# Performance work log

Measured on AMD Instinct MI355X. Metric: run time of the kernel, lower is better.

Reference implementation:

```python
import jax, jax.numpy as jnp
import numpy as np

DIM = 384
HEADS = 6
HEAD_DIM = DIM // HEADS
MLP_DIM = int(DIM * 4.0)
EPS = 1e-5


def layer_norm(x, g, b):
    mu = jnp.mean(x, axis=-1, keepdims=True)
    var = jnp.mean(jnp.square(x - mu), axis=-1, keepdims=True)
    return (x - mu) * jax.lax.rsqrt(var + EPS) * g + b


def setup_inputs() -> dict:
    key = jax.random.key(0)
    ks = jax.random.split(key, 12)
    s = 0.02
    return {
        "x": jax.random.normal(ks[0], (8, 2048, DIM), dtype=jnp.float32),
        "ln1_g": jnp.ones((DIM,), jnp.float32),
        "ln1_b": jnp.zeros((DIM,), jnp.float32),
        "qkv_w": jax.random.normal(ks[1], (DIM, 3 * DIM), jnp.float32) * s,
        "qkv_b": jnp.zeros((3 * DIM,), jnp.float32),
        "proj_w": jax.random.normal(ks[2], (DIM, DIM), jnp.float32) * s,
        "proj_b": jnp.zeros((DIM,), jnp.float32),
        "ln2_g": jnp.ones((DIM,), jnp.float32),
        "ln2_b": jnp.zeros((DIM,), jnp.float32),
        "fc1_w": jax.random.normal(ks[3], (DIM, MLP_DIM), jnp.float32) * s,
        "fc1_b": jnp.zeros((MLP_DIM,), jnp.float32),
        "fc2_w": jax.random.normal(ks[4], (MLP_DIM, DIM), jnp.float32) * s,
        "fc2_b": jnp.zeros((DIM,), jnp.float32),
    }


def reference(x, ln1_g, ln1_b, qkv_w, qkv_b, proj_w, proj_b,
              ln2_g, ln2_b, fc1_w, fc1_b, fc2_w, fc2_b):
    B, N, C = x.shape
    # --- attention ---
    h = layer_norm(x, ln1_g, ln1_b)
    qkv = h @ qkv_w + qkv_b  # [B,N,3C]
    qkv = qkv.reshape(B, N, 3, HEADS, HEAD_DIM)
    q, k, v = jnp.moveaxis(qkv, 2, 0)  # each [B,N,H,D]
    scale = HEAD_DIM ** -0.5
    attn = jnp.einsum('bnhd,bmhd->bhnm', q, k) * scale  # [B,H,N,N]
    attn = jax.nn.softmax(attn, axis=-1)
    o = jnp.einsum('bhnm,bmhd->bnhd', attn, v).reshape(B, N, C)
    x = x + o @ proj_w + proj_b
    # --- mlp ---
    h = layer_norm(x, ln2_g, ln2_b)
    h = jax.nn.gelu(h @ fc1_w + fc1_b, approximate=False)
    x = x + h @ fc2_w + fc2_b
    return x
```

## Files before the change

kernel.cpp:

```cpp
#include <hip/hip_runtime.h>
#include <hip/hip_bf16.h>

#define DIM   384
#define SEQ   2048
#define BATCH 8
#define NHEAD 6
#define HD    64
#define MLPD  1536
#define MTOT  (BATCH*SEQ)

typedef __attribute__((ext_vector_type(8))) short bf16x8;
typedef __attribute__((ext_vector_type(4))) float f32x4;

static __device__ __forceinline__ float bf2f(unsigned short u){
    union { float f; unsigned int i; } v; v.i = ((unsigned int)u) << 16; return v.f;
}
static __device__ __forceinline__ unsigned short f2bf(float f){
    union { float f; unsigned int i; } v; v.f = f;
    unsigned int r = v.i + 0x7fffu + ((v.i >> 16) & 1u);
    return (unsigned short)(r >> 16);
}
static __device__ __forceinline__ unsigned int asu(float f){
    union { float f; unsigned int i; } v; v.f = f; return v.i;
}
static __device__ __forceinline__ void gload_lds16(const unsigned short* g, unsigned short* l){
    __builtin_amdgcn_global_load_lds(
        (__attribute__((address_space(1))) void*)(g),
        (__attribute__((address_space(3))) void*)(l), 16, 0, 0);
}

__global__ __launch_bounds__(256) void wt_all_kernel(
    const float* __restrict__ qkv_w, const float* __restrict__ proj_w,
    const float* __restrict__ fc1_w, const float* __restrict__ fc2_w,
    unsigned short* __restrict__ o_qkv, unsigned short* __restrict__ o_prj,
    unsigned short* __restrict__ o_fc1, unsigned short* __restrict__ o_fc2)
{
    __shared__ float tile[64][68];
    int bid = blockIdx.x;
    const float* W; unsigned short* Wt; int K, N, tk, tn;
    if (bid < 108)      { W = qkv_w; Wt = o_qkv; K = 384;  N = 1152; tk = bid/18;        tn = bid%18; }
    else if (bid < 144) { W = proj_w; Wt = o_prj; K = 384;  N = 384;  tk = (bid-108)/6;  tn = (bid-108)%6; }
    else if (bid < 288) { W = fc1_w; Wt = o_fc1; K = 384;  N = 1536; tk = (bid-144)/24; tn = (bid-144)%24; }
    else                { W = fc2_w; Wt = o_fc2; K = 1536; N = 384;  tk = (bid-288)/6;  tn = (bid-288)%6; }
    int t = threadIdx.x;
    int lr = t >> 4, lc = (t & 15) * 4;
#pragma unroll
    for (int p = 0; p < 4; p++){
        float4 v = *(const float4*)(W + (size_t)(tk*64 + p*16 + lr) * N + tn*64 + lc);
        *(float4*)&tile[p*16 + lr][lc] = v;
    }
    __syncthreads();
    int n = t >> 2, k0 = (t & 3) * 16;
    unsigned int w[8];
#pragma unroll
    for (int i = 0; i < 8; i++)
        w[i] = (unsigned int)f2bf(tile[k0 + 2*i][n]) | ((unsigned int)f2bf(tile[k0 + 2*i + 1][n]) << 16);
    unsigned short* dst = Wt + (size_t)(tn*64 + n) * K + tk*64 + k0;
    *(uint4*)(dst)     = make_uint4(w[0], w[1], w[2], w[3]);
    *(uint4*)(dst + 8) = make_uint4(w[4], w[5], w[6], w[7]);
}

__global__ __launch_bounds__(256) void vt_kernel(const unsigned short* __restrict__ vtmp,
                                                 unsigned short* __restrict__ vb){
    __shared__ unsigned short tile[64][72];
    int bh = blockIdx.y, ns0 = blockIdx.x * 64;
    const unsigned short* src = vtmp + ((size_t)bh * SEQ + ns0) * 64;
    int t = threadIdx.x;
#pragma unroll
    for (int p = 0; p < 2; p++){
        int idx = t + p * 256;
        int r = idx >> 3, c = (idx & 7) * 8;
        *(uint4*)&tile[r][c] = *(const uint4*)(src + (size_t)r * 64 + c);
    }
    __syncthreads();
    int d = t >> 2, j0 = (t & 3) * 16;
    unsigned int w[8];
#pragma unroll
    for (int m = 0; m < 8; m++)
        w[m] = (unsigned int)tile[j0 + 2*m][d] | ((unsigned int)tile[j0 + 2*m + 1][d] << 16);
    unsigned short* dst = vb + ((size_t)bh * 64 + d) * SEQ + ns0 + j0;
    *(uint4*)(dst)     = make_uint4(w[0], w[1], w[2], w[3]);
    *(uint4*)(dst + 8) = make_uint4(w[4], w[5], w[6], w[7]);
}

__global__ __launch_bounds__(256) void ln_kernel(const float* __restrict__ x,
                                                 const float* __restrict__ g,
                                                 const float* __restrict__ b,
                                                 unsigned short* __restrict__ out){
    int row  = blockIdx.x * 4 + (threadIdx.x >> 6);
    int lane = threadIdx.x & 63;
    const float* xr = x + (size_t)row * DIM;
    float v[6];
#pragma unroll
    for (int p = 0; p < 3; p++){
        float2 t = *(const float2*)(xr + lane * 2 + p * 128);
        v[2*p] = t.x; v[2*p+1] = t.y;
    }
    float s = 0.f, sq = 0.f;
#pragma unroll
    for (int i = 0; i < 6; i++){ s += v[i]; sq += v[i] * v[i]; }
#pragma unroll
    for (int off = 1; off < 64; off <<= 1){
        s  += __shfl_xor(s, off);
        sq += __shfl_xor(sq, off);
    }
    float mu   = s * (1.0f / DIM);
    float var  = sq * (1.0f / DIM) - mu * mu;
    float rstd = rsqrtf(var + 1e-5f);
    unsigned short* orow = out + (size_t)row * DIM;
#pragma unroll
    for (int p = 0; p < 3; p++){
        int c = lane * 2 + p * 128;
        float h0 = (v[2*p]   - mu) * rstd * g[c]   + b[c];
        float h1 = (v[2*p+1] - mu) * rstd * g[c+1] + b[c+1];
        unsigned int pk = (unsigned int)f2bf(h0) | ((unsigned int)f2bf(h1) << 16);
        *(unsigned int*)(orow + c) = pk;
    }
}

template<int EPI, int BN>
__global__ __launch_bounds__(256) void gemm_kernel(
    const unsigned short* __restrict__ A, const unsigned short* __restrict__ Bt,
    const float* __restrict__ bias, int K, int N,
    const float* __restrict__ resid, float* __restrict__ outf,
    unsigned short* __restrict__ outb,
    unsigned short* __restrict__ qb, unsigned short* __restrict__ kb2,
    unsigned short* __restrict__ vb)
{
    constexpr int FI = (BN == 128) ? 4 : 2;
    constexpr int WROWS = (BN == 128) ? 64 : 32;
    __shared__ __align__(16) unsigned short As[128 * 64];
    __shared__ __align__(16) unsigned short Bs[BN * 64];
    int t = threadIdx.x;
    int wid = t >> 6, lane = t & 63, quad = lane >> 4, l15 = lane & 15;
    int wr = (BN == 128) ? (wid >> 1) : wid;
    int wc = (BN == 128) ? (wid & 1) : 0;
    int row0 = blockIdx.y * 128, col0 = blockIdx.x * BN;
    int sr = lane >> 3, sc = lane & 7;
    int scl = (sc ^ sr) * 8;

    const unsigned short* Ab = A  + (size_t)row0 * K;
    const unsigned short* Bb = Bt + (size_t)col0 * K;

    f32x4 acc[FI][4];
    f32x4 zz = {0.f, 0.f, 0.f, 0.f};
#pragma unroll
    for (int i = 0; i < FI; i++)
#pragma unroll
        for (int j = 0; j < 4; j++) acc[i][j] = zz;

    for (int k0 = 0; k0 < K; k0 += 64){
        __syncthreads();
#pragma unroll
        for (int j = 0; j < 4; j++){
            int rb = wid * 32 + j * 8;
            gload_lds16(Ab + (size_t)(rb + sr) * K + k0 + scl, &As[rb * 64]);
            if (BN == 128){
                gload_lds16(Bb + (size_t)(rb + sr) * K + k0 + scl, &Bs[rb * 64]);
            } else if (j < 2){
                int rb2 = wid * 16 + j * 8;
                gload_lds16(Bb + (size_t)(rb2 + sr) * K + k0 + scl, &Bs[rb2 * 64]);
            }
        }
        __syncthreads();
#pragma unroll
        for (int kk = 0; kk < 2; kk++){
            bf16x8 af[FI], bf[4];
#pragma unroll
            for (int i = 0; i < FI; i++){
                int r = wr*WROWS + i*16 + l15;
                af[i] = *(const bf16x8*)&As[r * 64 + (((kk*4 + quad) ^ (l15 & 7)) * 8)];
            }
#pragma unroll
            for (int j = 0; j < 4; j++){
                int r = wc*64 + j*16 + l15;
                bf[j] = *(const bf16x8*)&Bs[r * 64 + (((kk*4 + quad) ^ (l15 & 7)) * 8)];
            }
#pragma unroll
            for (int i = 0; i < FI; i++)
#pragma unroll
                for (int j = 0; j < 4; j++)
                    acc[i][j] = __builtin_amdgcn_mfma_f32_16x16x32_bf16(af[i], bf[j], acc[i][j], 0, 0, 0);
        }
    }

#pragma unroll
    for (int i = 0; i < FI; i++){
#pragma unroll
        for (int j = 0; j < 4; j++){
            int gr0 = row0 + wr*WROWS + i*16 + quad*4;
            int gc  = col0 + wc*64 + j*16 + l15;
            float bia = bias[gc];
#pragma unroll
            for (int r = 0; r < 4; r++){
                int gr = gr0 + r;
                float val = acc[i][j][r] + bia;
                if (EPI == 1){
                    outf[(size_t)gr * N + gc] = resid[(size_t)gr * N + gc] + val;
                } else if (EPI == 2){
                    float u = val * (1.0f + 0.044715f * val * val);
                    float e = __builtin_amdgcn_exp2f(u * 2.3025851f);
                    outb[(size_t)gr * N + gc] = f2bf(val * e / (e + 1.0f));
                } else {
                    int trip = gc / 384, rem = gc - trip * 384;
                    int head = rem >> 6, d = rem & 63;
                    int bidx = gr >> 11, ns = gr & 2047;
                    size_t off = ((size_t)(bidx * NHEAD + head) * SEQ + ns) * 64 + d;
                    unsigned short* dst = (trip == 0) ? qb : (trip == 1) ? kb2 : vb;
                    dst[off] = f2bf(val);
                }
            }
        }
    }
}

__global__ __launch_bounds__(128, 3) void attn_kernel(const unsigned short* __restrict__ Q,
                                                      const unsigned short* __restrict__ Kb,
                                                      const unsigned short* __restrict__ Vt,
                                                      unsigned short* __restrict__ O){
    __shared__ __align__(16) unsigned short Ks[64 * 64];
    __shared__ __align__(16) unsigned short Vs[64 * 64];
    __shared__ __align__(16) unsigned short Ps[2][32 * 64];

    int bh = blockIdx.y, qt = blockIdx.x;
    int t = threadIdx.x, wid = t >> 6, lane = t & 63, quad = lane >> 4, l15 = lane & 15;
    int l7 = l15 & 7;
    int q0 = qt * 64 + wid * 32;
    const unsigned short* Qp = Q  + (size_t)bh * SEQ * 64;
    const unsigned short* Kp = Kb + (size_t)bh * SEQ * 64;
    const unsigned short* Vp = Vt + (size_t)bh * 64 * SEQ;
    int sr = lane >> 3, sc = lane & 7;
    int scl = (sc ^ sr) * 8;

    const float QSCALE = 0.125f * 1.44269504f;
    bf16x8 qf[2][2];
#pragma unroll
    for (int h = 0; h < 2; h++){
#pragma unroll
        for (int c = 0; c < 2; c++){
            union { uint4 u; unsigned short s[8]; } cv;
            cv.u = *(const uint4*)(Qp + (size_t)(q0 + h*16 + l15) * 64 + c * 32 + quad * 8);
            bf16x8 f;
#pragma unroll
            for (int j = 0; j < 8; j++) f[j] = (short)f2bf(bf2f(cv.s[j]) * QSCALE);
            qf[h][c] = f;
        }
    }

    bf16x8 ones;
#pragma unroll
    for (int j = 0; j < 8; j++) ones[j] = (short)0x3F80;

    f32x4 oacc[2][4], sacc[2];
    f32x4 zz = {0.f, 0.f, 0.f, 0.f};
#pragma unroll
    for (int h = 0; h < 2; h++){
        sacc[h] = zz;
#pragma unroll
        for (int dn = 0; dn < 4; dn++) oacc[h][dn] = zz;
    }
    unsigned short* P = &Ps[wid][0];

    const unsigned short* kf_ptr[4][2];
#pragma unroll
    for (int n = 0; n < 4; n++){
        int kv = n * 16 + l15;
        kf_ptr[n][0] = &Ks[kv * 64 + ((quad       ^ (kv & 7)) * 8)];
        kf_ptr[n][1] = &Ks[kv * 64 + (((4 + quad) ^ (kv & 7)) * 8)];
    }
    const unsigned short* vf_ptr[2][4];
#pragma unroll
    for (int c = 0; c < 2; c++)
#pragma unroll
        for (int dn = 0; dn < 4; dn++){
            int d = dn * 16 + l15;
            vf_ptr[c][dn] = &Vs[d * 64 + (((c*4 + quad) ^ (d & 7)) * 8)];
        }
    const unsigned short* pf_ptr[2][2];
#pragma unroll
    for (int c = 0; c < 2; c++)
#pragma unroll
        for (int h = 0; h < 2; h++)
            pf_ptr[c][h] = P + (h*16 + l15) * 64 + (((c*4 + quad) ^ l7) * 8);
    uint2* pw_ptr[2][4];
#pragma unroll
    for (int h = 0; h < 2; h++)
#pragma unroll
        for (int n = 0; n < 4; n++){
            int qloc = h * 16 + l15;
            int chunk = n * 2 + (quad >> 1);
            pw_ptr[h][n] = (uint2*)(P + qloc * 64 + ((chunk ^ l7) * 8) + (quad & 1) * 4);
        }
    const unsigned short* kstage[4];
    const unsigned short* vstage[4];
    unsigned short* klds[4];
    unsigned short* vlds[4];
#pragma unroll
    for (int jj = 0; jj < 4; jj++){
        int rb = wid * 32 + jj * 8;
        kstage[jj] = Kp + (size_t)(rb + sr) * 64 + scl;
        vstage[jj] = Vp + (size_t)(rb + sr) * SEQ + scl;
        klds[jj] = &Ks[rb * 64];
        vlds[jj] = &Vs[rb * 64];
    }

    for (int kt = 0; kt < SEQ / 64; kt++){
        __syncthreads();
#pragma unroll
        for (int jj = 0; jj < 4; jj++){
            gload_lds16(kstage[jj], klds[jj]);
            gload_lds16(vstage[jj], vlds[jj]);
            kstage[jj] += 64 * 64;
            vstage[jj] += 64;
        }
        __syncthreads();

        f32x4 st[2][4];
#pragma unroll
        for (int n = 0; n < 4; n++){
            bf16x8 kf0 = *(const bf16x8*)kf_ptr[n][0];
            bf16x8 kf1 = *(const bf16x8*)kf_ptr[n][1];
#pragma unroll
            for (int h = 0; h < 2; h++){
                f32x4 z = __builtin_amdgcn_mfma_f32_16x16x32_bf16(kf0, qf[h][0], zz, 0, 0, 0);
                st[h][n] = __builtin_amdgcn_mfma_f32_16x16x32_bf16(kf1, qf[h][1], z, 0, 0, 0);
            }
        }

#pragma unroll
        for (int h = 0; h < 2; h++){
#pragma unroll
            for (int n = 0; n < 4; n++){
                float p0 = __builtin_amdgcn_exp2f(st[h][n][0]);
                float p1 = __builtin_amdgcn_exp2f(st[h][n][1]);
                float p2 = __builtin_amdgcn_exp2f(st[h][n][2]);
                float p3 = __builtin_amdgcn_exp2f(st[h][n][3]);
                unsigned int w0 = __builtin_amdgcn_perm(asu(p1), asu(p0), 0x07060302u);
                unsigned int w1 = __builtin_amdgcn_perm(asu(p3), asu(p2), 0x07060302u);
                *pw_ptr[h][n] = make_uint2(w0, w1);
            }
        }

        asm volatile("s_waitcnt lgkmcnt(0)" ::: "memory");

#pragma unroll
        for (int c = 0; c < 2; c++){
            bf16x8 pf[2];
#pragma unroll
            for (int h = 0; h < 2; h++)
                pf[h] = *(const bf16x8*)pf_ptr[c][h];
            sacc[0] = __builtin_amdgcn_mfma_f32_16x16x32_bf16(ones, pf[0], sacc[0], 0, 0, 0);
            sacc[1] = __builtin_amdgcn_mfma_f32_16x16x32_bf16(ones, pf[1], sacc[1], 0, 0, 0);
#pragma unroll
            for (int dn = 0; dn < 4; dn++){
                bf16x8 vf = *(const bf16x8*)vf_ptr[c][dn];
                oacc[0][dn] = __builtin_amdgcn_mfma_f32_16x16x32_bf16(vf, pf[0], oacc[0][dn], 0, 0, 0);
                oacc[1][dn] = __builtin_amdgcn_mfma_f32_16x16x32_bf16(vf, pf[1], oacc[1][dn], 0, 0, 0);
            }
        }
    }

    int b = bh / NHEAD, hh = bh - b * NHEAD;
#pragma unroll
    for (int h = 0; h < 2; h++){
        float rd = 1.0f / sacc[h][0];
        size_t row = (size_t)(b * SEQ + q0 + h*16 + l15);
#pragma unroll
        for (int dn = 0; dn < 4; dn++){
            float v0 = oacc[h][dn][0] * rd, v1 = oacc[h][dn][1] * rd;
            float v2 = oacc[h][dn][2] * rd, v3 = oacc[h][dn][3] * rd;
            unsigned int w0 = (unsigned int)f2bf(v0) | ((unsigned int)f2bf(v1) << 16);
            unsigned int w1 = (unsigned int)f2bf(v2) | ((unsigned int)f2bf(v3) << 16);
            *(uint2*)(O + row * DIM + hh * 64 + dn * 16 + quad * 4) = make_uint2(w0, w1);
        }
    }
}

extern "C" void kernel_launch(void* const* d_in, const int* in_sizes, int n_in,
                              void* d_out, int out_size, void* d_ws, size_t ws_size,
                              hipStream_t stream){
    const float* x      = (const float*)d_in[0];
    const float* ln1_g  = (const float*)d_in[1];
    const float* ln1_b  = (const float*)d_in[2];
    const float* qkv_w  = (const float*)d_in[3];
    const float* qkv_b  = (const float*)d_in[4];
    const float* proj_w = (const float*)d_in[5];
    const float* proj_b = (const float*)d_in[6];
    const float* ln2_g  = (const float*)d_in[7];
    const float* ln2_b  = (const float*)d_in[8];
    const float* fc1_w  = (const float*)d_in[9];
    const float* fc1_b  = (const float*)d_in[10];
    const float* fc2_w  = (const float*)d_in[11];
    const float* fc2_b  = (const float*)d_in[12];
    float* out = (float*)d_out;

    char* p = (char*)d_ws;
    auto take = [&](size_t n){ char* r = p; p += (n + 255) & ~(size_t)255; return r; };
    unsigned short* wt_qkv = (unsigned short*)take((size_t)1152 * 384 * 2);
    unsigned short* wt_prj = (unsigned short*)take((size_t)384 * 384 * 2);
    unsigned short* wt_fc1 = (unsigned short*)take((size_t)1536 * 384 * 2);
    unsigned short* wt_fc2 = (unsigned short*)take((size_t)384 * 1536 * 2);
    unsigned short* rbig   = (unsigned short*)take((size_t)MTOT * 4 * DIM * 2);
    unsigned short* h2     = (unsigned short*)take((size_t)MTOT * DIM * 2);
    float*          x1     = (float*)take((size_t)MTOT * DIM * 4);

    unsigned short* h1     = rbig;
    unsigned short* qb     = rbig + (size_t)MTOT * DIM;
    unsigned short* kb     = qb   + (size_t)MTOT * DIM;
    unsigned short* vb     = kb   + (size_t)MTOT * DIM;
    unsigned short* vtmp   = h2;
    unsigned short* attn_o = rbig;
    unsigned short* hm     = rbig;

    wt_all_kernel<<<dim3(432), 256, 0, stream>>>(qkv_w, proj_w, fc1_w, fc2_w,
                                                 wt_qkv, wt_prj, wt_fc1, wt_fc2);
    ln_kernel<<<dim3(MTOT/4), 256, 0, stream>>>(x, ln1_g, ln1_b, h1);
    gemm_kernel<0,128><<<dim3(9, 128), 256, 0, stream>>>(h1, wt_qkv, qkv_b, 384, 1152,
                                                         nullptr, nullptr, nullptr, qb, kb, vtmp);
    vt_kernel<<<dim3(SEQ/64, BATCH*NHEAD), 256, 0, stream>>>(vtmp, vb);
    attn_kernel<<<dim3(SEQ/64, BATCH*NHEAD), 128, 0, stream>>>(qb, kb, vb, attn_o);
    gemm_kernel<1,64><<<dim3(6, 128), 256, 0, stream>>>(attn_o, wt_prj, proj_b, 384, 384,
                                                        x, x1, nullptr, nullptr, nullptr, nullptr);
    ln_kernel<<<dim3(MTOT/4), 256, 0, stream>>>(x1, ln2_g, ln2_b, h2);
    gemm_kernel<2,128><<<dim3(12, 128), 256, 0, stream>>>(h2, wt_fc1, fc1_b, 384, 1536,
                                                          nullptr, nullptr, hm, nullptr, nullptr, nullptr);
    gemm_kernel<1,64><<<dim3(6, 128), 256, 0, stream>>>(hm, wt_fc2, fc2_b, 1536, 384,
                                                        x1, out, nullptr, nullptr, nullptr, nullptr);
}
```

Before: 329.5 us.

## Fuse V transpose into QKV GEMM epilogue and retile GEMMs to 64x128

Removes the separate vt_kernel by having QKV GEMM blocks that cover V columns stage their output in shared memory transposed and write it directly in [bh][d][seq] layout. All GEMMs are retiled to 64x128 tiles with 128-thread blocks and launch bounds of 3 blocks per CU, each wave computing 32x128. This saves one kernel launch plus a full round trip of V through global memory, at the cost of higher register use per thread and smaller blocks.

```diff
diff --git a/kernel.cpp b/kernel.cpp
--- a/kernel.cpp
+++ b/kernel.cpp
@@ -60,29 +60,6 @@
     *(uint4*)(dst + 8) = make_uint4(w[4], w[5], w[6], w[7]);
 }
 
-__global__ __launch_bounds__(256) void vt_kernel(const unsigned short* __restrict__ vtmp,
-                                                 unsigned short* __restrict__ vb){
-    __shared__ unsigned short tile[64][72];
-    int bh = blockIdx.y, ns0 = blockIdx.x * 64;
-    const unsigned short* src = vtmp + ((size_t)bh * SEQ + ns0) * 64;
-    int t = threadIdx.x;
-#pragma unroll
-    for (int p = 0; p < 2; p++){
-        int idx = t + p * 256;
-        int r = idx >> 3, c = (idx & 7) * 8;
-        *(uint4*)&tile[r][c] = *(const uint4*)(src + (size_t)r * 64 + c);
-    }
-    __syncthreads();
-    int d = t >> 2, j0 = (t & 3) * 16;
-    unsigned int w[8];
-#pragma unroll
-    for (int m = 0; m < 8; m++)
-        w[m] = (unsigned int)tile[j0 + 2*m][d] | ((unsigned int)tile[j0 + 2*m + 1][d] << 16);
-    unsigned short* dst = vb + ((size_t)bh * 64 + d) * SEQ + ns0 + j0;
-    *(uint4*)(dst)     = make_uint4(w[0], w[1], w[2], w[3]);
-    *(uint4*)(dst + 8) = make_uint4(w[4], w[5], w[6], w[7]);
-}
-
 __global__ __launch_bounds__(256) void ln_kernel(const float* __restrict__ x,
                                                  const float* __restrict__ g,
                                                  const float* __restrict__ b,
@@ -118,8 +95,8 @@
     }
 }
 
-template<int EPI, int BN>
-__global__ __launch_bounds__(256) void gemm_kernel(
+template<int EPI>
+__global__ __launch_bounds__(128, 3) void gemm_kernel(
     const unsigned short* __restrict__ A, const unsigned short* __restrict__ Bt,
     const float* __restrict__ bias, int K, int N,
     const float* __restrict__ resid, float* __restrict__ outf,
@@ -127,69 +104,91 @@
     unsigned short* __restrict__ qb, unsigned short* __restrict__ kb2,
     unsigned short* __restrict__ vb)
 {
-    constexpr int FI = (BN == 128) ? 4 : 2;
-    constexpr int WROWS = (BN == 128) ? 64 : 32;
-    __shared__ __align__(16) unsigned short As[128 * 64];
-    __shared__ __align__(16) unsigned short Bs[BN * 64];
+    __shared__ __align__(16) unsigned short smem[64*64 + 128*64];
+    unsigned short* As = smem;
+    unsigned short* Bs = smem + 64*64;
     int t = threadIdx.x;
     int wid = t >> 6, lane = t & 63, quad = lane >> 4, l15 = lane & 15;
-    int wr = (BN == 128) ? (wid >> 1) : wid;
-    int wc = (BN == 128) ? (wid & 1) : 0;
-    int row0 = blockIdx.y * 128, col0 = blockIdx.x * BN;
+    int row0 = blockIdx.y * 64, col0 = blockIdx.x * 128;
     int sr = lane >> 3, sc = lane & 7;
     int scl = (sc ^ sr) * 8;
 
     const unsigned short* Ab = A  + (size_t)row0 * K;
     const unsigned short* Bb = Bt + (size_t)col0 * K;
 
-    f32x4 acc[FI][4];
+    f32x4 acc[2][8];
     f32x4 zz = {0.f, 0.f, 0.f, 0.f};
 #pragma unroll
-    for (int i = 0; i < FI; i++)
-#pragma unroll
-        for (int j = 0; j < 4; j++) acc[i][j] = zz;
+    for (int i = 0; i < 2; i++)
+#pragma unroll
+        for (int j = 0; j < 8; j++) acc[i][j] = zz;
 
     for (int k0 = 0; k0 < K; k0 += 64){
         __syncthreads();
 #pragma unroll
-        for (int j = 0; j < 4; j++){
-            int rb = wid * 32 + j * 8;
+        for (int jj = 0; jj < 4; jj++){
+            int rb = wid * 32 + jj * 8;
             gload_lds16(Ab + (size_t)(rb + sr) * K + k0 + scl, &As[rb * 64]);
-            if (BN == 128){
-                gload_lds16(Bb + (size_t)(rb + sr) * K + k0 + scl, &Bs[rb * 64]);
-            } else if (j < 2){
-                int rb2 = wid * 16 + j * 8;
-                gload_lds16(Bb + (size_t)(rb2 + sr) * K + k0 + scl, &Bs[rb2 * 64]);
-            }
+        }
+#pragma unroll
+        for (int jj = 0; jj < 8; jj++){
+            int rb = wid * 64 + jj * 8;
+            gload_lds16(Bb + (size_t)(rb + sr) * K + k0 + scl, &Bs[rb * 64]);
         }
         __syncthreads();
 #pragma unroll
         for (int kk = 0; kk < 2; kk++){
-            bf16x8 af[FI], bf[4];
-#pragma unroll
-            for (int i = 0; i < FI; i++){
-                int r = wr*WROWS + i*16 + l15;
+            bf16x8 af[2], bf[8];
+#pragma unroll
+            for (int i = 0; i < 2; i++){
+                int r = wid*32 + i*16 + l15;
                 af[i] = *(const bf16x8*)&As[r * 64 + (((kk*4 + quad) ^ (l15 & 7)) * 8)];
             }
 #pragma unroll
-            for (int j = 0; j < 4; j++){
-                int r = wc*64 + j*16 + l15;
+            for (int j = 0; j < 8; j++){
+                int r = j*16 + l15;
                 bf[j] = *(const bf16x8*)&Bs[r * 64 + (((kk*4 + quad) ^ (l15 & 7)) * 8)];
             }
 #pragma unroll
-            for (int i = 0; i < FI; i++)
-#pragma unroll
-                for (int j = 0; j < 4; j++)
+            for (int i = 0; i < 2; i++)
+#pragma unroll
+                for (int j = 0; j < 8; j++)
                     acc[i][j] = __builtin_amdgcn_mfma_f32_16x16x32_bf16(af[i], bf[j], acc[i][j], 0, 0, 0);
         }
     }
 
-#pragma unroll
-    for (int i = 0; i < FI; i++){
-#pragma unroll
-        for (int j = 0; j < 4; j++){
-            int gr0 = row0 + wr*WROWS + i*16 + quad*4;
-            int gc  = col0 + wc*64 + j*16 + l15;
+    if (EPI == 0 && col0 >= 768){
+        __syncthreads();
+        unsigned short* T = smem;
+#pragma unroll
+        for (int i = 0; i < 2; i++)
+#pragma unroll
+            for (int j = 0; j < 8; j++){
+                int gcl = j*16 + l15;
+                float bia = bias[col0 + gcl];
+                int nsl0 = wid*32 + i*16 + quad*4;
+#pragma unroll
+                for (int r = 0; r < 4; r++)
+                    T[gcl * 72 + nsl0 + r] = f2bf(acc[i][j][r] + bia);
+            }
+        __syncthreads();
+        int rem = (col0 - 768) + t;
+        int head = rem >> 6, d = rem & 63;
+        int bidx = row0 >> 11, ns0 = row0 & 2047;
+        unsigned short* dst = vb + ((size_t)((bidx * NHEAD + head) * 64 + d)) * SEQ + ns0;
+        const unsigned short* src = T + t * 72;
+#pragma unroll
+        for (int m = 0; m < 8; m++)
+            *(uint4*)(dst + m*8) = *(const uint4*)(src + m*8);
+        return;
+    }
+
+#pragma unroll
+    for (int i = 0; i < 2; i++){
+#pragma unroll
+        for (int j = 0; j < 8; j++){
+            int gr0 = row0 + wid*32 + i*16 + quad*4;
+            int gc  = col0 + j*16 + l15;
             float bia = bias[gc];
 #pragma unroll
             for (int r = 0; r < 4; r++){
@@ -202,12 +201,12 @@
                     float e = __builtin_amdgcn_exp2f(u * 2.3025851f);
                     outb[(size_t)gr * N + gc] = f2bf(val * e / (e + 1.0f));
                 } else {
-                    int trip = gc / 384, rem = gc - trip * 384;
-                    int head = rem >> 6, d = rem & 63;
+                    int trip = gc / 384, remq = gc - trip * 384;
+                    int head = remq >> 6, d = remq & 63;
                     int bidx = gr >> 11, ns = gr & 2047;
                     size_t off = ((size_t)(bidx * NHEAD + head) * SEQ + ns) * 64 + d;
-                    unsigned short* dst = (trip == 0) ? qb : (trip == 1) ? kb2 : vb;
-                    dst[off] = f2bf(val);
+                    unsigned short* dstp = (trip == 0) ? qb : kb2;
+                    dstp[off] = f2bf(val);
                 }
             }
         }
@@ -408,22 +407,20 @@
     unsigned short* qb     = rbig + (size_t)MTOT * DIM;
     unsigned short* kb     = qb   + (size_t)MTOT * DIM;
     unsigned short* vb     = kb   + (size_t)MTOT * DIM;
-    unsigned short* vtmp   = h2;
     unsigned short* attn_o = rbig;
     unsigned short* hm     = rbig;
 
     wt_all_kernel<<<dim3(432), 256, 0, stream>>>(qkv_w, proj_w, fc1_w, fc2_w,
                                                  wt_qkv, wt_prj, wt_fc1, wt_fc2);
     ln_kernel<<<dim3(MTOT/4), 256, 0, stream>>>(x, ln1_g, ln1_b, h1);
-    gemm_kernel<0,128><<<dim3(9, 128), 256, 0, stream>>>(h1, wt_qkv, qkv_b, 384, 1152,
-                                                         nullptr, nullptr, nullptr, qb, kb, vtmp);
-    vt_kernel<<<dim3(SEQ/64, BATCH*NHEAD), 256, 0, stream>>>(vtmp, vb);
+    gemm_kernel<0><<<dim3(9, 256), 128, 0, stream>>>(h1, wt_qkv, qkv_b, 384, 1152,
+                                                     nullptr, nullptr, nullptr, qb, kb, vb);
     attn_kernel<<<dim3(SEQ/64, BATCH*NHEAD), 128, 0, stream>>>(qb, kb, vb, attn_o);
-    gemm_kernel<1,64><<<dim3(6, 128), 256, 0, stream>>>(attn_o, wt_prj, proj_b, 384, 384,
-                                                        x, x1, nullptr, nullptr, nullptr, nullptr);
+    gemm_kernel<1><<<dim3(3, 256), 128, 0, stream>>>(attn_o, wt_prj, proj_b, 384, 384,
+                                                     x, x1, nullptr, nullptr, nullptr, nullptr);
     ln_kernel<<<dim3(MTOT/4), 256, 0, stream>>>(x1, ln2_g, ln2_b, h2);
-    gemm_kernel<2,128><<<dim3(12, 128), 256, 0, stream>>>(h2, wt_fc1, fc1_b, 384, 1536,
-                                                          nullptr, nullptr, hm, nullptr, nullptr, nullptr);
-    gemm_kernel<1,64><<<dim3(6, 128), 256, 0, stream>>>(hm, wt_fc2, fc2_b, 1536, 384,
-                                                        x1, out, nullptr, nullptr, nullptr, nullptr);
-}
+    gemm_kernel<2><<<dim3(12, 256), 128, 0, stream>>>(h2, wt_fc1, fc1_b, 384, 1536,
+                                                      nullptr, nullptr, hm, nullptr, nullptr, nullptr);
+    gemm_kernel<1><<<dim3(3, 256), 128, 0, stream>>>(hm, wt_fc2, fc2_b, 1536, 384,
+                                                     x1, out, nullptr, nullptr, nullptr, nullptr);
+}
```

Measured after the change: 310.7 us. -5.7%, faster.
